# Optimization experiments

Hardware: AMD Instinct MI355X
Metric: run time of the kernel (lower is better)

## Reference

```python
import jax, jax.numpy as jnp
import numpy as np

N_NODES = 50000
N_EDGES = 800000
N_ENT = 500000
N_REL = 500
L = 2          # num_layers
H = 8          # head_num
D = 16         # per-head dim (hidden_dim // head_num)
HID = H * D    # 128
IN = 128       # in_ent_dim == in_rel_dim == hidden_dim
B = 64         # number of graphs in the batch
SLOPE = 0.2    # leaky-relu negative slope


def setup_inputs() -> dict:
    key = jax.random.key(0)
    ks = jax.random.split(key, 11)
    return {
        "ent_table": jax.random.normal(ks[0], (N_ENT, IN), jnp.float32) * 0.05,
        "rel_table": jax.random.normal(ks[1], (N_REL, IN), jnp.float32) * 0.05,
        "W_ent": jax.random.normal(ks[2], (L, IN, HID), jnp.float32) * 0.05,
        "W_rel": jax.random.normal(ks[3], (L, IN, HID), jnp.float32) * 0.05,
        "attn_l": jax.random.normal(ks[4], (L, H, D), jnp.float32) * 0.05,
        "attn_r": jax.random.normal(ks[5], (L, H, D), jnp.float32) * 0.05,
        "attn_e": jax.random.normal(ks[6], (L, H, D), jnp.float32) * 0.05,
        "ent_ids": jax.random.randint(ks[7], (N_NODES,), 0, N_ENT, jnp.int32),
        "rel_ids": jax.random.randint(ks[8], (N_EDGES,), 0, N_REL, jnp.int32),
        "src": jax.random.randint(ks[9], (N_EDGES,), 0, N_NODES, jnp.int32),
        "dst": jax.random.randint(ks[10], (N_EDGES,), 0, N_NODES, jnp.int32),
        # node-0 offset of each subgraph in the batched graph
        "graph_offsets": jnp.arange(B, dtype=jnp.int32) * (N_NODES // B),
    }


def _kge_layer(h, rel_f, src, dst, W_e, W_r, a_l, a_r, a_e):
    # GAT-style relation-aware message passing (KGELayer)
    feat = (h @ W_e).reshape(-1, H, D)        # [N,H,D]
    rfeat = (rel_f @ W_r).reshape(-1, H, D)   # [E,H,D]
    el = jnp.einsum('nhd,hd->nh', feat, a_l)  # src score
    er = jnp.einsum('nhd,hd->nh', feat, a_r)  # dst score
    ee = jnp.einsum('ehd,hd->eh', rfeat, a_e) # relation score
    e = jax.nn.leaky_relu(el[src] + er[dst] + ee, SLOPE)  # [E,H]
    # segment softmax over incoming edges of each dst node
    emax = jax.ops.segment_max(e, dst, num_segments=N_NODES)
    ex = jnp.exp(e - emax[dst])
    denom = jax.ops.segment_sum(ex, dst, num_segments=N_NODES)
    alpha = ex / denom[dst]                   # [E,H]
    msg = (feat[src] + rfeat) * alpha[:, :, None]  # [E,H,D]
    out = jax.ops.segment_sum(msg, dst, num_segments=N_NODES)  # [N,H,D]
    return out.reshape(-1, HID)


def reference(ent_table, rel_table, W_ent, W_rel, attn_l, attn_r, attn_e,
              ent_ids, rel_ids, src, dst, graph_offsets):
    h = ent_table[ent_ids]       # [N,IN]
    rel_f = rel_table[rel_ids]   # [E,IN]
    for l in range(L):
        h = _kge_layer(h, rel_f, src, dst, W_ent[l], W_rel[l],
                       attn_l[l], attn_r[l], attn_e[l])
    # CLS embedding: node 0 of each unbatched subgraph
    return h[graph_offsets]      # [B,HID]
```

## Files before the change

### kernel.cpp

```cpp
#include <hip/hip_runtime.h>
#include <hip/hip_bf16.h>


#define NN   50000
#define NE   800000
#define NR   500
#define HH   8
#define DD   16
#define HIDD 128
#define BB   64

#define MAXE2 16384
#define MAXS1 16448
#define MAXE1 262144
#define MAXS0 50000


__global__ void k_init(int* slot2, int* slot1, int* slot0, int* counters,
                       float* out2, float* den2) {
    int i = blockIdx.x * blockDim.x + threadIdx.x;
    int stride = gridDim.x * blockDim.x;
    for (int n = i; n < NN; n += stride) { slot2[n] = -1; slot1[n] = -1; slot0[n] = -1; }
    for (int n = i; n < BB * HIDD; n += stride) out2[n] = 0.f;
    for (int n = i; n < BB * HH; n += stride) den2[n] = 0.f;
    if (i < 8) counters[i] = 0;
}

__global__ void k_seed(const int* goffs, int* slot2, int* slot1, int* nodesS1,
                       int* counters) {
    int i = threadIdx.x;
    if (i < BB) {
        int n = goffs[i];
        slot2[n] = i;
        slot1[n] = -2;
        nodesS1[i] = n;
    }
    if (i == 0) counters[0] = BB;
}

#define EBUF 1024
#define NBUF 512
__global__ void k_scan(const int* __restrict__ src, const int* __restrict__ dst,
                       const int* __restrict__ slotHit, int* __restrict__ slotNew,
                       int* elist, int elistCap, int* nodes, int nodesCap,
                       int* counters, int cntE, int cntN) {
    __shared__ int lE[EBUF];
    __shared__ int lN[NBUF];
    __shared__ int cEsh, cNsh, baseE, baseN;
    if (threadIdx.x == 0) { cEsh = 0; cNsh = 0; }
    __syncthreads();
    int per = (NE + gridDim.x - 1) / gridDim.x;
    int lo = blockIdx.x * per;
    int hi = lo + per; if (hi > NE) hi = NE;
    for (int base = lo; base < hi; base += blockDim.x) {
        int e = base + threadIdx.x;
        if (e < hi) {
            int d = dst[e];
            if (slotHit[d] >= 0) {
                int pos = atomicAdd(&cEsh, 1);
                lE[pos] = e;
                int s = src[e];
                int old = atomicCAS(&slotNew[s], -1, -2);
                if (old == -1) {
                    int p2 = atomicAdd(&cNsh, 1);
                    lN[p2] = s;
                }
            }
        }
        __syncthreads();
        if (cEsh >= EBUF - 256 || cNsh >= NBUF - 256) {
            int nE = cEsh, nN = cNsh;
            if (threadIdx.x == 0) {
                baseE = atomicAdd(&counters[cntE], nE);
                baseN = atomicAdd(&counters[cntN], nN);
            }
            __syncthreads();
            for (int i = threadIdx.x; i < nE; i += blockDim.x) {
                int g = baseE + i; if (g < elistCap) elist[g] = lE[i];
            }
            for (int i = threadIdx.x; i < nN; i += blockDim.x) {
                int g = baseN + i; if (g < nodesCap) nodes[g] = lN[i];
            }
            __syncthreads();
            if (threadIdx.x == 0) { cEsh = 0; cNsh = 0; }
        }
        __syncthreads();
    }
    int nE = cEsh, nN = cNsh;
    if (threadIdx.x == 0) {
        baseE = atomicAdd(&counters[cntE], nE);
        baseN = atomicAdd(&counters[cntN], nN);
    }
    __syncthreads();
    for (int i = threadIdx.x; i < nE; i += blockDim.x) {
        int g = baseE + i; if (g < elistCap) elist[g] = lE[i];
    }
    for (int i = threadIdx.x; i < nN; i += blockDim.x) {
        int g = baseN + i; if (g < nodesCap) nodes[g] = lN[i];
    }
}

__global__ void k_finS1(int* slot1, const int* nodesS1, int* slot0, int* nodesS0,
                        int* counters) {
    int k = blockIdx.x * blockDim.x + threadIdx.x;
    int cnt = counters[0]; if (cnt > MAXS1) cnt = MAXS1;
    if (k < cnt) {
        int n = nodesS1[k];
        slot1[n] = k;
        slot0[n] = -2;
        nodesS0[k] = n;
    }
    if (k == 0) counters[1] = cnt;
}

__global__ void k_zeroS1(const int* counters, float* h1acc, float* den1) {
    int cnt = counters[0]; if (cnt > MAXS1) cnt = MAXS1;
    int i = blockIdx.x * blockDim.x + threadIdx.x;
    int stride = gridDim.x * blockDim.x;
    for (int n = i; n < cnt * HIDD; n += stride) h1acc[n] = 0.f;
    for (int n = i; n < cnt * HH; n += stride) den1[n] = 0.f;
}

__global__ void k_finS0(int* slot0, const int* nodesS0, const int* counters) {
    int k = blockIdx.x * blockDim.x + threadIdx.x;
    int cnt = counters[1]; if (cnt > MAXS0) cnt = MAXS0;
    if (k < cnt) slot0[nodesS0[k]] = k;
}

__global__ void k_rel(const float* rel_table, const float* __restrict__ W_rel,
                      const float* attn_e, float* rproj, float* ee) {
    int b = blockIdx.x;
    int l = b / NR, r = b % NR;
    int t = threadIdx.x;
    __shared__ float row[HIDD];
    __shared__ float rp[HIDD];
    row[t] = rel_table[r * HIDD + t];
    __syncthreads();
    const float* W = W_rel + l * HIDD * HIDD;
    float acc = 0.f;
    for (int j = 0; j < HIDD; j++) acc += row[j] * W[j * HIDD + t];
    rproj[(l * NR + r) * HIDD + t] = acc;
    rp[t] = acc;
    __syncthreads();
    if (t < HH) {
        float s = 0.f;
        for (int d = 0; d < DD; d++) s += rp[t * DD + d] * attn_e[(l * HH + t) * DD + d];
        ee[(l * NR + r) * HH + t] = s;
    }
}

#define FT 8
__global__ void k_feat0(const int* nodesS0, const int* counters, const int* ent_ids,
                        const float* __restrict__ ent_table, const float* __restrict__ W_ent,
                        const float* __restrict__ attn_l, const float* __restrict__ attn_r,
                        float* feat0, float* el0, float* er0) {
    int t = threadIdx.x;
    int cnt = counters[1]; if (cnt > MAXS0) cnt = MAXS0;
    __shared__ float rows[FT][HIDD];
    int nTiles = (cnt + FT - 1) / FT;
    for (int tile = blockIdx.x; tile < nTiles; tile += gridDim.x) {
        int k0 = tile * FT;
        #pragma unroll
        for (int m = 0; m < FT; m++) {
            int k = k0 + m;
            int n = nodesS0[k < cnt ? k : 0];
            rows[m][t] = ent_table[(long)ent_ids[n] * HIDD + t];
        }
        __syncthreads();
        float acc[FT];
        #pragma unroll
        for (int m = 0; m < FT; m++) acc[m] = 0.f;
        for (int j = 0; j < HIDD; j++) {
            float w = W_ent[j * HIDD + t];
            #pragma unroll
            for (int m = 0; m < FT; m++) acc[m] += rows[m][j] * w;
        }
        __syncthreads();
        #pragma unroll
        for (int m = 0; m < FT; m++) {
            int k = k0 + m;
            if (k < cnt) feat0[k * HIDD + t] = acc[m];
            rows[m][t] = acc[m];
        }
        __syncthreads();
        {
            int m = t >> 4, idx = t & 15, h = idx >> 1, isR = idx & 1;
            int k = k0 + m;
            if (k < cnt) {
                const float* av = (isR ? attn_r : attn_l) + h * DD;
                float s = 0.f;
                for (int d = 0; d < DD; d++) s += rows[m][h * DD + d] * av[d];
                if (isR) er0[k * HH + h] = s; else el0[k * HH + h] = s;
            }
        }
        __syncthreads();
    }
}

__global__ void k_score1(const int* e1list, const int* counters,
                         const int* src, const int* dst, const int* rel_ids,
                         const int* slot0, const int* slot1,
                         const float* el0, const float* er0, const float* ee0,
                         float* ex1, float* den1) {
    int i = blockIdx.x * blockDim.x + threadIdx.x;
    int stride = gridDim.x * blockDim.x;
    int cnt = counters[3]; if (cnt > MAXE1) cnt = MAXE1;
    int total = cnt * HH;
    for (; i < total; i += stride) {
        int eidx = i >> 3, h = i & 7;
        int e = e1list[eidx];
        int ks  = slot0[src[e]];
        int kd0 = slot0[dst[e]];
        int kd1 = slot1[dst[e]];
        int rid = rel_ids[e];
        float sc = el0[ks * HH + h] + er0[kd0 * HH + h] + ee0[rid * HH + h];
        sc = sc >= 0.f ? sc : 0.2f * sc;
        float ex = expf(sc);
        ex1[eidx * HH + h] = ex;
        atomicAdd(&den1[kd1 * HH + h], ex);
    }
}

__global__ void k_msg1(const int* e1list, const int* counters,
                       const int* src, const int* dst, const int* rel_ids,
                       const int* slot0, const int* slot1,
                       const float* __restrict__ feat0, const float* __restrict__ rproj0,
                       const float* __restrict__ ex1, float* h1acc) {
    int i = blockIdx.x * blockDim.x + threadIdx.x;
    int stride = gridDim.x * blockDim.x;
    int cnt = counters[3]; if (cnt > MAXE1) cnt = MAXE1;
    int total = cnt * HIDD;
    for (; i < total; i += stride) {
        int eidx = i >> 7, col = i & 127;
        int e = e1list[eidx];
        int ks  = slot0[src[e]];
        int kd  = slot1[dst[e]];
        int rid = rel_ids[e];
        float ex = ex1[eidx * HH + (col >> 4)];
        float v = (feat0[ks * HIDD + col] + rproj0[rid * HIDD + col]) * ex;
        atomicAdd(&h1acc[kd * HIDD + col], v);
    }
}

__global__ void k_feat1(const int* counters, const float* h1acc, const float* den1,
                        const float* __restrict__ W_ent1,
                        const float* attn_l1, const float* attn_r1,
                        float* feat1, float* el1, float* er1) {
    int t = threadIdx.x;
    int cnt = counters[0]; if (cnt > MAXS1) cnt = MAXS1;
    __shared__ float row[HIDD];
    __shared__ float f[HIDD];
    for (int k = blockIdx.x; k < cnt; k += gridDim.x) {
        float den = den1[k * HH + (t >> 4)];
        row[t] = den > 0.f ? h1acc[k * HIDD + t] / den : 0.f;
        __syncthreads();
        float acc = 0.f;
        for (int j = 0; j < HIDD; j++) acc += row[j] * W_ent1[j * HIDD + t];
        feat1[k * HIDD + t] = acc;
        f[t] = acc;
        __syncthreads();
        if (t < HH) {
            float s = 0.f;
            for (int d = 0; d < DD; d++) s += f[t * DD + d] * attn_l1[t * DD + d];
            el1[k * HH + t] = s;
        } else if (t < 2 * HH) {
            int h = t - HH;
            float s = 0.f;
            for (int d = 0; d < DD; d++) s += f[h * DD + d] * attn_r1[h * DD + d];
            er1[k * HH + h] = s;
        }
        __syncthreads();
    }
}

__global__ void k_score2(const int* e2list, const int* counters,
                         const int* src, const int* dst, const int* rel_ids,
                         const int* slot1, const int* slot2,
                         const float* el1, const float* er1, const float* ee1,
                         float* ex2, float* den2) {
    int i = blockIdx.x * blockDim.x + threadIdx.x;
    int stride = gridDim.x * blockDim.x;
    int cnt = counters[2]; if (cnt > MAXE2) cnt = MAXE2;
    int total = cnt * HH;
    for (; i < total; i += stride) {
        int eidx = i >> 3, h = i & 7;
        int e = e2list[eidx];
        int ks  = slot1[src[e]];
        int kd1 = slot1[dst[e]];
        int g   = slot2[dst[e]];
        int rid = rel_ids[e];
        float sc = el1[ks * HH + h] + er1[kd1 * HH + h] + ee1[rid * HH + h];
        sc = sc >= 0.f ? sc : 0.2f * sc;
        float ex = expf(sc);
        ex2[eidx * HH + h] = ex;
        atomicAdd(&den2[g * HH + h], ex);
    }
}

__global__ void k_msg2(const int* e2list, const int* counters,
                       const int* src, const int* dst, const int* rel_ids,
                       const int* slot1, const int* slot2,
                       const float* feat1, const float* rproj1, const float* ex2,
                       float* out2) {
    int i = blockIdx.x * blockDim.x + threadIdx.x;
    int stride = gridDim.x * blockDim.x;
    int cnt = counters[2]; if (cnt > MAXE2) cnt = MAXE2;
    int total = cnt * HIDD;
    for (; i < total; i += stride) {
        int eidx = i >> 7, col = i & 127;
        int e = e2list[eidx];
        int ks  = slot1[src[e]];
        int g   = slot2[dst[e]];
        int rid = rel_ids[e];
        float ex = ex2[eidx * HH + (col >> 4)];
        float v = (feat1[ks * HIDD + col] + rproj1[rid * HIDD + col]) * ex;
        atomicAdd(&out2[g * HIDD + col], v);
    }
}

__global__ void k_out(const float* out2, const float* den2, float* out) {
    int i = blockIdx.x * blockDim.x + threadIdx.x;
    if (i >= BB * HIDD) return;
    int g = i >> 7, col = i & 127;
    float den = den2[g * HH + (col >> 4)];
    out[i] = den > 0.f ? out2[i] / den : 0.f;
}

extern "C" void kernel_launch(void* const* d_in, const int* in_sizes, int n_in,
                              void* d_out, int out_size, void* d_ws, size_t ws_size,
                              hipStream_t stream) {
    const float* ent_table = (const float*)d_in[0];
    const float* rel_table = (const float*)d_in[1];
    const float* W_ent     = (const float*)d_in[2];
    const float* W_rel     = (const float*)d_in[3];
    const float* attn_l    = (const float*)d_in[4];
    const float* attn_r    = (const float*)d_in[5];
    const float* attn_e    = (const float*)d_in[6];
    const int*   ent_ids   = (const int*)d_in[7];
    const int*   rel_ids   = (const int*)d_in[8];
    const int*   src       = (const int*)d_in[9];
    const int*   dst       = (const int*)d_in[10];
    const int*   goffs     = (const int*)d_in[11];
    float*       out       = (float*)d_out;

    char* p = (char*)d_ws;
    auto alloc = [&](size_t nbytes) {
        void* q = (void*)p;
        p += (nbytes + 255) & ~(size_t)255;
        return q;
    };
    float* rproj   = (float*)alloc((size_t)2 * NR * HIDD * 4);
    float* ee      = (float*)alloc((size_t)2 * NR * HH * 4);
    int*   slot2   = (int*)alloc((size_t)NN * 4);
    int*   slot1   = (int*)alloc((size_t)NN * 4);
    int*   slot0   = (int*)alloc((size_t)NN * 4);
    int*   nodesS1 = (int*)alloc((size_t)MAXS1 * 4);
    int*   nodesS0 = (int*)alloc((size_t)MAXS0 * 4);
    int*   e2list  = (int*)alloc((size_t)MAXE2 * 4);
    int*   e1list  = (int*)alloc((size_t)MAXE1 * 4);
    int*   counters= (int*)alloc(8 * 4);
    float* feat0   = (float*)alloc((size_t)MAXS0 * HIDD * 4);
    float* el0     = (float*)alloc((size_t)MAXS0 * HH * 4);
    float* er0     = (float*)alloc((size_t)MAXS0 * HH * 4);
    float* ex1     = (float*)alloc((size_t)MAXE1 * HH * 4);
    float* h1acc   = (float*)alloc((size_t)MAXS1 * HIDD * 4);
    float* den1    = (float*)alloc((size_t)MAXS1 * HH * 4);
    float* feat1   = (float*)alloc((size_t)MAXS1 * HIDD * 4);
    float* el1     = (float*)alloc((size_t)MAXS1 * HH * 4);
    float* er1     = (float*)alloc((size_t)MAXS1 * HH * 4);
    float* ex2     = (float*)alloc((size_t)MAXE2 * HH * 4);
    float* out2    = (float*)alloc((size_t)BB * HIDD * 4);
    float* den2    = (float*)alloc((size_t)BB * HH * 4);

    const float* rproj0 = rproj;
    const float* rproj1 = rproj + (size_t)NR * HIDD;
    const float* ee0 = ee;
    const float* ee1 = ee + (size_t)NR * HH;
    const float* W_ent0 = W_ent;
    const float* W_ent1 = W_ent + HIDD * HIDD;
    const float* attn_l0 = attn_l, *attn_l1 = attn_l + HH * DD;
    const float* attn_r0 = attn_r, *attn_r1 = attn_r + HH * DD;

    hipLaunchKernelGGL(k_init, dim3(256), dim3(256), 0, stream,
                       slot2, slot1, slot0, counters, out2, den2);
    hipLaunchKernelGGL(k_seed, dim3(1), dim3(64), 0, stream,
                       goffs, slot2, slot1, nodesS1, counters);
    hipLaunchKernelGGL(k_scan, dim3(512), dim3(256), 0, stream,
                       src, dst, slot2, slot1, e2list, MAXE2, nodesS1, MAXS1,
                       counters, 2, 0);
    hipLaunchKernelGGL(k_finS1, dim3((MAXS1 + 255) / 256), dim3(256), 0, stream,
                       slot1, nodesS1, slot0, nodesS0, counters);
    hipLaunchKernelGGL(k_zeroS1, dim3(256), dim3(256), 0, stream,
                       counters, h1acc, den1);
    hipLaunchKernelGGL(k_scan, dim3(512), dim3(256), 0, stream,
                       src, dst, slot1, slot0, e1list, MAXE1, nodesS0, MAXS0,
                       counters, 3, 1);
    hipLaunchKernelGGL(k_finS0, dim3((MAXS0 + 255) / 256), dim3(256), 0, stream,
                       slot0, nodesS0, counters);
    hipLaunchKernelGGL(k_rel, dim3(2 * NR), dim3(HIDD), 0, stream,
                       rel_table, W_rel, attn_e, rproj, ee);
    hipLaunchKernelGGL(k_feat0, dim3(1024), dim3(HIDD), 0, stream,
                       nodesS0, counters, ent_ids, ent_table, W_ent0,
                       attn_l0, attn_r0, feat0, el0, er0);
    hipLaunchKernelGGL(k_score1, dim3(512), dim3(256), 0, stream,
                       e1list, counters, src, dst, rel_ids, slot0, slot1,
                       el0, er0, ee0, ex1, den1);
    hipLaunchKernelGGL(k_msg1, dim3(2048), dim3(256), 0, stream,
                       e1list, counters, src, dst, rel_ids, slot0, slot1,
                       feat0, rproj0, ex1, h1acc);
    hipLaunchKernelGGL(k_feat1, dim3(512), dim3(HIDD), 0, stream,
                       counters, h1acc, den1, W_ent1, attn_l1, attn_r1,
                       feat1, el1, er1);
    hipLaunchKernelGGL(k_score2, dim3(256), dim3(256), 0, stream,
                       e2list, counters, src, dst, rel_ids, slot1, slot2,
                       el1, er1, ee1, ex2, den2);
    hipLaunchKernelGGL(k_msg2, dim3(256), dim3(256), 0, stream,
                       e2list, counters, src, dst, rel_ids, slot1, slot2,
                       feat1, rproj1, ex2, out2);
    hipLaunchKernelGGL(k_out, dim3((BB * HIDD + 255) / 256), dim3(256), 0, stream,
                       out2, den2, out);
}
```

Measured before the change: 426.0 us.

## Build per-destination CSR and replace atomic scatter with pull-based fused layers

```diff
diff --git a/kernel.cpp b/kernel.cpp
--- a/kernel.cpp
+++ b/kernel.cpp
@@ -10,24 +10,23 @@
 #define HIDD 128
 #define BB   64
 
+#define GRIDS 1024
+#define PER   784
+
 #define MAXE2 16384
 #define MAXS1 16448
 #define MAXE1 262144
 #define MAXS0 50000
 
 
-__global__ void k_init(int* slot2, int* slot1, int* slot0, int* counters,
-                       float* out2, float* den2) {
+__global__ void k_init(int* slot2, int* slot1, int* slot0, int* counters) {
     int i = blockIdx.x * blockDim.x + threadIdx.x;
     int stride = gridDim.x * blockDim.x;
     for (int n = i; n < NN; n += stride) { slot2[n] = -1; slot1[n] = -1; slot0[n] = -1; }
-    for (int n = i; n < BB * HIDD; n += stride) out2[n] = 0.f;
-    for (int n = i; n < BB * HH; n += stride) den2[n] = 0.f;
     if (i < 8) counters[i] = 0;
 }
 
-__global__ void k_seed(const int* goffs, int* slot2, int* slot1, int* nodesS1,
-                       int* counters) {
+__global__ void k_seed(const int* goffs, int* slot2, int* slot1, int* nodesS1) {
     int i = threadIdx.x;
     if (i < BB) {
         int n = goffs[i];
@@ -35,130 +34,235 @@
         slot1[n] = -2;
         nodesS1[i] = n;
     }
-    if (i == 0) counters[0] = BB;
-}
-
-#define EBUF 1024
-#define NBUF 512
+}
+
 __global__ void k_scan(const int* __restrict__ src, const int* __restrict__ dst,
                        const int* __restrict__ slotHit, int* __restrict__ slotNew,
-                       int* elist, int elistCap, int* nodes, int nodesCap,
-                       int* counters, int cntE, int cntN) {
-    __shared__ int lE[EBUF];
-    __shared__ int lN[NBUF];
-    __shared__ int cEsh, cNsh, baseE, baseN;
-    if (threadIdx.x == 0) { cEsh = 0; cNsh = 0; }
-    __syncthreads();
-    int per = (NE + gridDim.x - 1) / gridDim.x;
-    int lo = blockIdx.x * per;
-    int hi = lo + per; if (hi > NE) hi = NE;
-    for (int base = lo; base < hi; base += blockDim.x) {
-        int e = base + threadIdx.x;
-        if (e < hi) {
-            int d = dst[e];
-            if (slotHit[d] >= 0) {
-                int pos = atomicAdd(&cEsh, 1);
-                lE[pos] = e;
-                int s = src[e];
-                int old = atomicCAS(&slotNew[s], -1, -2);
-                if (old == -1) {
-                    int p2 = atomicAdd(&cNsh, 1);
-                    lN[p2] = s;
-                }
+                       int* eseg, int* ecnt, int* nseg, int* ncnt) {
+    __shared__ int cE, cN;
+    if (threadIdx.x == 0) { cE = 0; cN = 0; }
+    __syncthreads();
+    int b = blockIdx.x;
+    int lo = b * PER;
+    int hi = lo + PER; if (hi > NE) hi = NE;
+    int* es = eseg + (size_t)b * PER;
+    int* ns = nseg + (size_t)b * PER;
+    for (int e = lo + threadIdx.x; e < hi; e += blockDim.x) {
+        int d = dst[e];
+        if (slotHit[d] >= 0) {
+            int pos = atomicAdd(&cE, 1);
+            es[pos] = e;
+            int s = src[e];
+            if (atomicCAS(&slotNew[s], -1, -2) == -1) {
+                int p = atomicAdd(&cN, 1);
+                ns[p] = s;
             }
         }
-        __syncthreads();
-        if (cEsh >= EBUF - 256 || cNsh >= NBUF - 256) {
-            int nE = cEsh, nN = cNsh;
-            if (threadIdx.x == 0) {
-                baseE = atomicAdd(&counters[cntE], nE);
-                baseN = atomicAdd(&counters[cntN], nN);
-            }
-            __syncthreads();
-            for (int i = threadIdx.x; i < nE; i += blockDim.x) {
-                int g = baseE + i; if (g < elistCap) elist[g] = lE[i];
-            }
-            for (int i = threadIdx.x; i < nN; i += blockDim.x) {
-                int g = baseN + i; if (g < nodesCap) nodes[g] = lN[i];
-            }
-            __syncthreads();
-            if (threadIdx.x == 0) { cEsh = 0; cNsh = 0; }
-        }
-        __syncthreads();
-    }
-    int nE = cEsh, nN = cNsh;
-    if (threadIdx.x == 0) {
-        baseE = atomicAdd(&counters[cntE], nE);
-        baseN = atomicAdd(&counters[cntN], nN);
-    }
-    __syncthreads();
-    for (int i = threadIdx.x; i < nE; i += blockDim.x) {
-        int g = baseE + i; if (g < elistCap) elist[g] = lE[i];
-    }
-    for (int i = threadIdx.x; i < nN; i += blockDim.x) {
-        int g = baseN + i; if (g < nodesCap) nodes[g] = lN[i];
-    }
-}
-
-__global__ void k_finS1(int* slot1, const int* nodesS1, int* slot0, int* nodesS0,
-                        int* counters) {
-    int k = blockIdx.x * blockDim.x + threadIdx.x;
-    int cnt = counters[0]; if (cnt > MAXS1) cnt = MAXS1;
-    if (k < cnt) {
-        int n = nodesS1[k];
-        slot1[n] = k;
-        slot0[n] = -2;
-        nodesS0[k] = n;
-    }
-    if (k == 0) counters[1] = cnt;
-}
-
-__global__ void k_zeroS1(const int* counters, float* h1acc, float* den1) {
-    int cnt = counters[0]; if (cnt > MAXS1) cnt = MAXS1;
+    }
+    __syncthreads();
+    if (threadIdx.x == 0) { ecnt[b] = cE; ncnt[b] = cN; }
+}
+
+__device__ int block_scan_counts(const int* cnts, int nblk, int* bases, int offset) {
+    __shared__ int part[256];
+    __shared__ int total_sh;
+    int t = threadIdx.x;
+    int per = (nblk + 255) / 256;
+    int s = 0;
+    for (int j = 0; j < per; j++) { int i = t * per + j; if (i < nblk) s += cnts[i]; }
+    part[t] = s;
+    __syncthreads();
+    for (int d = 1; d < 256; d <<= 1) {
+        int v = (t >= d) ? part[t - d] : 0;
+        __syncthreads();
+        part[t] += v;
+        __syncthreads();
+    }
+    int run = ((t == 0) ? 0 : part[t - 1]) + offset;
+    for (int j = 0; j < per; j++) {
+        int i = t * per + j;
+        if (i < nblk) { bases[i] = run; run += cnts[i]; }
+    }
+    if (t == 255) total_sh = part[255];
+    __syncthreads();
+    return total_sh;
+}
+
+__global__ void k_prefix2(const int* ecnt2, const int* ncnt2, int* ebase2, int* nbase2,
+                          int* counters, const int* nodesS1, int* slot1, int* slot0,
+                          int* nodesS0) {
+    int t = threadIdx.x;
+    int totE = block_scan_counts(ecnt2, GRIDS, ebase2, 0);
+    int totN = block_scan_counts(ncnt2, GRIDS, nbase2, BB);
+    if (t == 0) {
+        counters[2] = totE;
+        counters[0] = BB + totN;
+        counters[1] = BB + totN;
+    }
+    if (t < BB) {
+        int n = nodesS1[t];
+        slot1[n] = t;
+        slot0[n] = t;
+        nodesS0[t] = n;
+    }
+}
+
+__global__ void k_compact2(const int* eseg2, const int* ecnt2, const int* ebase2,
+                           const int* nseg2, const int* ncnt2, const int* nbase2,
+                           int* e2list, int* nodesS1, int* slot1, int* slot0,
+                           int* nodesS0, int* deg2) {
+    int b = blockIdx.x, t = threadIdx.x;
+    int ce = ecnt2[b], cn = ncnt2[b], be = ebase2[b], bn = nbase2[b];
+    const int* es = eseg2 + (size_t)b * PER;
+    const int* ns = nseg2 + (size_t)b * PER;
+    for (int i = t; i < ce; i += blockDim.x) {
+        int g = be + i; if (g < MAXE2) e2list[g] = es[i];
+    }
+    for (int i = t; i < cn; i += blockDim.x) {
+        int idx = bn + i;
+        if (idx < MAXS1) {
+            int n = ns[i];
+            nodesS1[idx] = n;
+            slot1[n] = idx;
+            slot0[n] = idx;
+            nodesS0[idx] = n;
+        }
+    }
+    if (b == 0) { for (int i = t; i < BB; i += blockDim.x) deg2[i] = 0; }
+}
+
+__global__ void k_prefix1(const int* ecnt1, const int* ncnt1, int* ebase1, int* nbase1,
+                          int* counters) {
+    int t = threadIdx.x;
+    int s0 = counters[1];
+    int totE = block_scan_counts(ecnt1, GRIDS, ebase1, 0);
+    int totN = block_scan_counts(ncnt1, GRIDS, nbase1, s0);
+    if (t == 0) {
+        counters[3] = totE;
+        counters[1] = s0 + totN;
+    }
+}
+
+__global__ void k_compact1(const int* eseg1, const int* ecnt1, const int* ebase1,
+                           const int* nseg1, const int* ncnt1, const int* nbase1,
+                           int* e1list, int* slot0, int* nodesS0,
+                           int* deg1, const int* counters) {
+    int b = blockIdx.x, t = threadIdx.x;
+    int ce = ecnt1[b], cn = ncnt1[b], be = ebase1[b], bn = nbase1[b];
+    const int* es = eseg1 + (size_t)b * PER;
+    const int* ns = nseg1 + (size_t)b * PER;
+    for (int i = t; i < ce; i += blockDim.x) {
+        int g = be + i; if (g < MAXE1) e1list[g] = es[i];
+    }
+    for (int i = t; i < cn; i += blockDim.x) {
+        int idx = bn + i;
+        if (idx < MAXS0) {
+            int n = ns[i];
+            slot0[n] = idx;
+            nodesS0[idx] = n;
+        }
+    }
+    int cnt1 = counters[0]; if (cnt1 > MAXS1) cnt1 = MAXS1;
+    for (int i = b * blockDim.x + t; i < cnt1; i += gridDim.x * blockDim.x) deg1[i] = 0;
+}
+
+__global__ void k_hist(const int* e2list, const int* e1list, const int* counters,
+                       const int* dst, const int* slot2, const int* slot1,
+                       int* deg2, int* deg1) {
     int i = blockIdx.x * blockDim.x + threadIdx.x;
     int stride = gridDim.x * blockDim.x;
-    for (int n = i; n < cnt * HIDD; n += stride) h1acc[n] = 0.f;
-    for (int n = i; n < cnt * HH; n += stride) den1[n] = 0.f;
-}
-
-__global__ void k_finS0(int* slot0, const int* nodesS0, const int* counters) {
-    int k = blockIdx.x * blockDim.x + threadIdx.x;
+    int c2 = counters[2]; if (c2 > MAXE2) c2 = MAXE2;
+    int c1 = counters[3]; if (c1 > MAXE1) c1 = MAXE1;
+    for (int k = i; k < c2; k += stride) atomicAdd(&deg2[slot2[dst[e2list[k]]]], 1);
+    for (int k = i; k < c1; k += stride) atomicAdd(&deg1[slot1[dst[e1list[k]]]], 1);
+}
+
+__device__ void excl_scan_glob(const int* deg, int n, int* rp) {
+    __shared__ int part[256];
+    int t = threadIdx.x;
+    int per = (n + 255) / 256;
+    int s = 0;
+    for (int j = 0; j < per; j++) { int i = t * per + j; if (i < n) s += deg[i]; }
+    part[t] = s;
+    __syncthreads();
+    for (int d = 1; d < 256; d <<= 1) {
+        int v = (t >= d) ? part[t - d] : 0;
+        __syncthreads();
+        part[t] += v;
+        __syncthreads();
+    }
+    int run = (t == 0) ? 0 : part[t - 1];
+    for (int j = 0; j < per; j++) {
+        int i = t * per + j;
+        if (i < n) { rp[i] = run; run += deg[i]; }
+    }
+    if (t == 255) rp[n] = part[255];
+    __syncthreads();
+}
+
+__global__ void k_rowptr(const int* deg2, const int* deg1, const int* counters,
+                         int* rp2, int* rp1, int* cur2, int* cur1) {
+    int t = threadIdx.x;
+    int cnt1 = counters[0]; if (cnt1 > MAXS1) cnt1 = MAXS1;
+    excl_scan_glob(deg2, BB, rp2);
+    excl_scan_glob(deg1, cnt1, rp1);
+    for (int i = t; i < BB; i += blockDim.x) cur2[i] = rp2[i];
+    for (int i = t; i < cnt1; i += blockDim.x) cur1[i] = rp1[i];
+}
+
+__global__ void k_scatter(const int* e2list, const int* e1list, const int* counters,
+                          const int* dst, const int* slot2, const int* slot1,
+                          int* cur2, int* cur1, int* csr2, int* csr1) {
+    int i = blockIdx.x * blockDim.x + threadIdx.x;
+    int stride = gridDim.x * blockDim.x;
+    int c2 = counters[2]; if (c2 > MAXE2) c2 = MAXE2;
+    int c1 = counters[3]; if (c1 > MAXE1) c1 = MAXE1;
+    for (int k = i; k < c2; k += stride) {
+        int e = e2list[k];
+        int pos = atomicAdd(&cur2[slot2[dst[e]]], 1);
+        if (pos < MAXE2) csr2[pos] = e;
+    }
+    for (int k = i; k < c1; k += stride) {
+        int e = e1list[k];
+        int pos = atomicAdd(&cur1[slot1[dst[e]]], 1);
+        if (pos < MAXE1) csr1[pos] = e;
+    }
+}
+
+#define FT 8
+__global__ void k_relfeat0(const float* rel_table, const float* __restrict__ W_rel,
+                           const float* attn_e, float* rproj, float* ee,
+                           const int* nodesS0, const int* counters, const int* ent_ids,
+                           const float* __restrict__ ent_table,
+                           const float* __restrict__ W_ent,
+                           const float* __restrict__ attn_l,
+                           const float* __restrict__ attn_r,
+                           float* feat0, float* el0, float* er0) {
+    __shared__ float rows[FT][HIDD];
+    int t = threadIdx.x;
+    if (blockIdx.x < 2 * NR) {
+        int l = blockIdx.x / NR, r = blockIdx.x % NR;
+        rows[0][t] = rel_table[r * HIDD + t];
+        __syncthreads();
+        const float* W = W_rel + l * HIDD * HIDD;
+        float acc = 0.f;
+        for (int j = 0; j < HIDD; j++) acc += rows[0][j] * W[j * HIDD + t];
+        rproj[(l * NR + r) * HIDD + t] = acc;
+        rows[1][t] = acc;
+        __syncthreads();
+        if (t < HH) {
+            float s = 0.f;
+            for (int d = 0; d < DD; d++)
+                s += rows[1][t * DD + d] * attn_e[(l * HH + t) * DD + d];
+            ee[(l * NR + r) * HH + t] = s;
+        }
+        return;
+    }
     int cnt = counters[1]; if (cnt > MAXS0) cnt = MAXS0;
-    if (k < cnt) slot0[nodesS0[k]] = k;
-}
-
-__global__ void k_rel(const float* rel_table, const float* __restrict__ W_rel,
-                      const float* attn_e, float* rproj, float* ee) {
-    int b = blockIdx.x;
-    int l = b / NR, r = b % NR;
-    int t = threadIdx.x;
-    __shared__ float row[HIDD];
-    __shared__ float rp[HIDD];
-    row[t] = rel_table[r * HIDD + t];
-    __syncthreads();
-    const float* W = W_rel + l * HIDD * HIDD;
-    float acc = 0.f;
-    for (int j = 0; j < HIDD; j++) acc += row[j] * W[j * HIDD + t];
-    rproj[(l * NR + r) * HIDD + t] = acc;
-    rp[t] = acc;
-    __syncthreads();
-    if (t < HH) {
-        float s = 0.f;
-        for (int d = 0; d < DD; d++) s += rp[t * DD + d] * attn_e[(l * HH + t) * DD + d];
-        ee[(l * NR + r) * HH + t] = s;
-    }
-}
-
-#define FT 8
-__global__ void k_feat0(const int* nodesS0, const int* counters, const int* ent_ids,
-                        const float* __restrict__ ent_table, const float* __restrict__ W_ent,
-                        const float* __restrict__ attn_l, const float* __restrict__ attn_r,
-                        float* feat0, float* el0, float* er0) {
-    int t = threadIdx.x;
-    int cnt = counters[1]; if (cnt > MAXS0) cnt = MAXS0;
-    __shared__ float rows[FT][HIDD];
+    int tile0 = blockIdx.x - 2 * NR;
+    int tstride = gridDim.x - 2 * NR;
     int nTiles = (cnt + FT - 1) / FT;
-    for (int tile = blockIdx.x; tile < nTiles; tile += gridDim.x) {
+    for (int tile = tile0; tile < nTiles; tile += tstride) {
         int k0 = tile * FT;
         #pragma unroll
         for (int m = 0; m < FT; m++) {
@@ -197,133 +301,77 @@
     }
 }
 
-__global__ void k_score1(const int* e1list, const int* counters,
-                         const int* src, const int* dst, const int* rel_ids,
-                         const int* slot0, const int* slot1,
-                         const float* el0, const float* er0, const float* ee0,
-                         float* ex1, float* den1) {
-    int i = blockIdx.x * blockDim.x + threadIdx.x;
-    int stride = gridDim.x * blockDim.x;
-    int cnt = counters[3]; if (cnt > MAXE1) cnt = MAXE1;
-    int total = cnt * HH;
-    for (; i < total; i += stride) {
-        int eidx = i >> 3, h = i & 7;
-        int e = e1list[eidx];
-        int ks  = slot0[src[e]];
-        int kd0 = slot0[dst[e]];
-        int kd1 = slot1[dst[e]];
-        int rid = rel_ids[e];
-        float sc = el0[ks * HH + h] + er0[kd0 * HH + h] + ee0[rid * HH + h];
-        sc = sc >= 0.f ? sc : 0.2f * sc;
-        float ex = expf(sc);
-        ex1[eidx * HH + h] = ex;
-        atomicAdd(&den1[kd1 * HH + h], ex);
-    }
-}
-
-__global__ void k_msg1(const int* e1list, const int* counters,
-                       const int* src, const int* dst, const int* rel_ids,
-                       const int* slot0, const int* slot1,
-                       const float* __restrict__ feat0, const float* __restrict__ rproj0,
-                       const float* __restrict__ ex1, float* h1acc) {
-    int i = blockIdx.x * blockDim.x + threadIdx.x;
-    int stride = gridDim.x * blockDim.x;
-    int cnt = counters[3]; if (cnt > MAXE1) cnt = MAXE1;
-    int total = cnt * HIDD;
-    for (; i < total; i += stride) {
-        int eidx = i >> 7, col = i & 127;
-        int e = e1list[eidx];
-        int ks  = slot0[src[e]];
-        int kd  = slot1[dst[e]];
-        int rid = rel_ids[e];
-        float ex = ex1[eidx * HH + (col >> 4)];
-        float v = (feat0[ks * HIDD + col] + rproj0[rid * HIDD + col]) * ex;
-        atomicAdd(&h1acc[kd * HIDD + col], v);
-    }
-}
-
-__global__ void k_feat1(const int* counters, const float* h1acc, const float* den1,
-                        const float* __restrict__ W_ent1,
-                        const float* attn_l1, const float* attn_r1,
-                        float* feat1, float* el1, float* er1) {
-    int t = threadIdx.x;
-    int cnt = counters[0]; if (cnt > MAXS1) cnt = MAXS1;
+__global__ void k_layer1(const int* counters, const int* rp1, const int* csr1,
+                         const int* src, const int* rel_ids, const int* slot0,
+                         const float* __restrict__ el0, const float* __restrict__ er0,
+                         const float* __restrict__ ee0,
+                         const float* __restrict__ feat0, const float* __restrict__ rproj0,
+                         const float* __restrict__ W_ent1,
+                         const float* attn_l1, const float* attn_r1,
+                         float* feat1, float* el1, float* er1) {
+    int cnt1 = counters[0]; if (cnt1 > MAXS1) cnt1 = MAXS1;
+    int t = threadIdx.x;
+    int h = t >> 4;
     __shared__ float row[HIDD];
-    __shared__ float f[HIDD];
-    for (int k = blockIdx.x; k < cnt; k += gridDim.x) {
-        float den = den1[k * HH + (t >> 4)];
-        row[t] = den > 0.f ? h1acc[k * HIDD + t] / den : 0.f;
-        __syncthreads();
-        float acc = 0.f;
-        for (int j = 0; j < HIDD; j++) acc += row[j] * W_ent1[j * HIDD + t];
-        feat1[k * HIDD + t] = acc;
-        f[t] = acc;
+    __shared__ float f2[HIDD];
+    for (int k = blockIdx.x; k < cnt1; k += gridDim.x) {
+        int lo = rp1[k], hi = rp1[k + 1];
+        float er_k = er0[k * HH + h];
+        float acc = 0.f, sumex = 0.f;
+        for (int i = lo; i < hi; i++) {
+            int e = csr1[i];
+            int ks = slot0[src[e]];
+            int rid = rel_ids[e];
+            float sc = el0[ks * HH + h] + er_k + ee0[rid * HH + h];
+            sc = sc >= 0.f ? sc : 0.2f * sc;
+            float ex = __expf(sc);
+            sumex += ex;
+            acc += ex * (feat0[ks * HIDD + t] + rproj0[rid * HIDD + t]);
+        }
+        row[t] = (hi > lo) ? acc / sumex : 0.f;
+        __syncthreads();
+        float f = 0.f;
+        for (int j = 0; j < HIDD; j++) f += row[j] * W_ent1[j * HIDD + t];
+        feat1[k * HIDD + t] = f;
+        f2[t] = f;
         __syncthreads();
         if (t < HH) {
             float s = 0.f;
-            for (int d = 0; d < DD; d++) s += f[t * DD + d] * attn_l1[t * DD + d];
+            for (int d = 0; d < DD; d++) s += f2[t * DD + d] * attn_l1[t * DD + d];
             el1[k * HH + t] = s;
         } else if (t < 2 * HH) {
-            int h = t - HH;
+            int hh = t - HH;
             float s = 0.f;
-            for (int d = 0; d < DD; d++) s += f[h * DD + d] * attn_r1[h * DD + d];
-            er1[k * HH + h] = s;
-        }
-        __syncthreads();
-    }
-}
-
-__global__ void k_score2(const int* e2list, const int* counters,
-                         const int* src, const int* dst, const int* rel_ids,
-                         const int* slot1, const int* slot2,
-                         const float* el1, const float* er1, const float* ee1,
-                         float* ex2, float* den2) {
-    int i = blockIdx.x * blockDim.x + threadIdx.x;
-    int stride = gridDim.x * blockDim.x;
-    int cnt = counters[2]; if (cnt > MAXE2) cnt = MAXE2;
-    int total = cnt * HH;
-    for (; i < total; i += stride) {
-        int eidx = i >> 3, h = i & 7;
-        int e = e2list[eidx];
-        int ks  = slot1[src[e]];
-        int kd1 = slot1[dst[e]];
-        int g   = slot2[dst[e]];
+            for (int d = 0; d < DD; d++) s += f2[hh * DD + d] * attn_r1[hh * DD + d];
+            er1[k * HH + hh] = s;
+        }
+        __syncthreads();
+    }
+}
+
+__global__ void k_layer2(const int* rp2, const int* csr2,
+                         const int* src, const int* rel_ids, const int* slot1,
+                         const float* __restrict__ el1, const float* __restrict__ er1,
+                         const float* __restrict__ ee1,
+                         const float* __restrict__ feat1, const float* __restrict__ rproj1,
+                         float* out) {
+    int g = blockIdx.x;
+    int t = threadIdx.x;
+    int h = t >> 4;
+    int lo = rp2[g], hi = rp2[g + 1];
+    float er_g = er1[g * HH + h];
+    float acc = 0.f, sumex = 0.f;
+    for (int i = lo; i < hi; i++) {
+        int e = csr2[i];
+        int ks = slot1[src[e]];
         int rid = rel_ids[e];
-        float sc = el1[ks * HH + h] + er1[kd1 * HH + h] + ee1[rid * HH + h];
+        float sc = el1[ks * HH + h] + er_g + ee1[rid * HH + h];
         sc = sc >= 0.f ? sc : 0.2f * sc;
-        float ex = expf(sc);
-        ex2[eidx * HH + h] = ex;
-        atomicAdd(&den2[g * HH + h], ex);
-    }
-}
-
-__global__ void k_msg2(const int* e2list, const int* counters,
-                       const int* src, const int* dst, const int* rel_ids,
-                       const int* slot1, const int* slot2,
-                       const float* feat1, const float* rproj1, const float* ex2,
-                       float* out2) {
-    int i = blockIdx.x * blockDim.x + threadIdx.x;
-    int stride = gridDim.x * blockDim.x;
-    int cnt = counters[2]; if (cnt > MAXE2) cnt = MAXE2;
-    int total = cnt * HIDD;
-    for (; i < total; i += stride) {
-        int eidx = i >> 7, col = i & 127;
-        int e = e2list[eidx];
-        int ks  = slot1[src[e]];
-        int g   = slot2[dst[e]];
-        int rid = rel_ids[e];
-        float ex = ex2[eidx * HH + (col >> 4)];
-        float v = (feat1[ks * HIDD + col] + rproj1[rid * HIDD + col]) * ex;
-        atomicAdd(&out2[g * HIDD + col], v);
-    }
-}
-
-__global__ void k_out(const float* out2, const float* den2, float* out) {
-    int i = blockIdx.x * blockDim.x + threadIdx.x;
-    if (i >= BB * HIDD) return;
-    int g = i >> 7, col = i & 127;
-    float den = den2[g * HH + (col >> 4)];
-    out[i] = den > 0.f ? out2[i] / den : 0.f;
+        float ex = __expf(sc);
+        sumex += ex;
+        acc += ex * (feat1[ks * HIDD + t] + rproj1[rid * HIDD + t]);
+    }
+    out[g * HIDD + t] = (hi > lo) ? acc / sumex : 0.f;
 }
 
 extern "C" void kernel_launch(void* const* d_in, const int* in_sizes, int n_in,
@@ -359,18 +407,32 @@
     int*   e2list  = (int*)alloc((size_t)MAXE2 * 4);
     int*   e1list  = (int*)alloc((size_t)MAXE1 * 4);
     int*   counters= (int*)alloc(8 * 4);
+    int*   eseg2   = (int*)alloc((size_t)GRIDS * PER * 4);
+    int*   nseg2   = (int*)alloc((size_t)GRIDS * PER * 4);
+    int*   eseg1   = (int*)alloc((size_t)GRIDS * PER * 4);
+    int*   nseg1   = (int*)alloc((size_t)GRIDS * PER * 4);
+    int*   ecnt2   = (int*)alloc((size_t)GRIDS * 4);
+    int*   ncnt2   = (int*)alloc((size_t)GRIDS * 4);
+    int*   ecnt1   = (int*)alloc((size_t)GRIDS * 4);
+    int*   ncnt1   = (int*)alloc((size_t)GRIDS * 4);
+    int*   ebase2  = (int*)alloc((size_t)GRIDS * 4);
+    int*   nbase2  = (int*)alloc((size_t)GRIDS * 4);
+    int*   ebase1  = (int*)alloc((size_t)GRIDS * 4);
+    int*   nbase1  = (int*)alloc((size_t)GRIDS * 4);
+    int*   deg2    = (int*)alloc((size_t)BB * 4);
+    int*   rp2     = (int*)alloc((size_t)(BB + 1) * 4);
+    int*   cur2    = (int*)alloc((size_t)BB * 4);
+    int*   deg1    = (int*)alloc((size_t)MAXS1 * 4);
+    int*   rp1     = (int*)alloc((size_t)(MAXS1 + 1) * 4);
+    int*   cur1    = (int*)alloc((size_t)MAXS1 * 4);
+    int*   csr2    = (int*)alloc((size_t)MAXE2 * 4);
+    int*   csr1    = (int*)alloc((size_t)MAXE1 * 4);
     float* feat0   = (float*)alloc((size_t)MAXS0 * HIDD * 4);
     float* el0     = (float*)alloc((size_t)MAXS0 * HH * 4);
     float* er0     = (float*)alloc((size_t)MAXS0 * HH * 4);
-    float* ex1     = (float*)alloc((size_t)MAXE1 * HH * 4);
-    float* h1acc   = (float*)alloc((size_t)MAXS1 * HIDD * 4);
-    float* den1    = (float*)alloc((size_t)MAXS1 * HH * 4);
     float* feat1   = (float*)alloc((size_t)MAXS1 * HIDD * 4);
     float* el1     = (float*)alloc((size_t)MAXS1 * HH * 4);
     float* er1     = (float*)alloc((size_t)MAXS1 * HH * 4);
-    float* ex2     = (float*)alloc((size_t)MAXE2 * HH * 4);
-    float* out2    = (float*)alloc((size_t)BB * HIDD * 4);
-    float* den2    = (float*)alloc((size_t)BB * HH * 4);
 
     const float* rproj0 = rproj;
     const float* rproj1 = rproj + (size_t)NR * HIDD;
@@ -382,41 +444,40 @@
     const float* attn_r0 = attn_r, *attn_r1 = attn_r + HH * DD;
 
     hipLaunchKernelGGL(k_init, dim3(256), dim3(256), 0, stream,
-                       slot2, slot1, slot0, counters, out2, den2);
+                       slot2, slot1, slot0, counters);
     hipLaunchKernelGGL(k_seed, dim3(1), dim3(64), 0, stream,
-                       goffs, slot2, slot1, nodesS1, counters);
-    hipLaunchKernelGGL(k_scan, dim3(512), dim3(256), 0, stream,
-                       src, dst, slot2, slot1, e2list, MAXE2, nodesS1, MAXS1,
-                       counters, 2, 0);
-    hipLaunchKernelGGL(k_finS1, dim3((MAXS1 + 255) / 256), dim3(256), 0, stream,
-                       slot1, nodesS1, slot0, nodesS0, counters);
-    hipLaunchKernelGGL(k_zeroS1, dim3(256), dim3(256), 0, stream,
-                       counters, h1acc, den1);
-    hipLaunchKernelGGL(k_scan, dim3(512), dim3(256), 0, stream,
-                       src, dst, slot1, slot0, e1list, MAXE1, nodesS0, MAXS0,
-                       counters, 3, 1);
-    hipLaunchKernelGGL(k_finS0, dim3((MAXS0 + 255) / 256), dim3(256), 0, stream,
-                       slot0, nodesS0, counters);
-    hipLaunchKernelGGL(k_rel, dim3(2 * NR), dim3(HIDD), 0, stream,
-                       rel_table, W_rel, attn_e, rproj, ee);
-    hipLaunchKernelGGL(k_feat0, dim3(1024), dim3(HIDD), 0, stream,
+                       goffs, slot2, slot1, nodesS1);
+    hipLaunchKernelGGL(k_scan, dim3(GRIDS), dim3(256), 0, stream,
+                       src, dst, slot2, slot1, eseg2, ecnt2, nseg2, ncnt2);
+    hipLaunchKernelGGL(k_prefix2, dim3(1), dim3(256), 0, stream,
+                       ecnt2, ncnt2, ebase2, nbase2, counters,
+                       nodesS1, slot1, slot0, nodesS0);
+    hipLaunchKernelGGL(k_compact2, dim3(GRIDS), dim3(256), 0, stream,
+                       eseg2, ecnt2, ebase2, nseg2, ncnt2, nbase2,
+                       e2list, nodesS1, slot1, slot0, nodesS0, deg2);
+    hipLaunchKernelGGL(k_scan, dim3(GRIDS), dim3(256), 0, stream,
+                       src, dst, slot1, slot0, eseg1, ecnt1, nseg1, ncnt1);
+    hipLaunchKernelGGL(k_prefix1, dim3(1), dim3(256), 0, stream,
+                       ecnt1, ncnt1, ebase1, nbase1, counters);
+    hipLaunchKernelGGL(k_compact1, dim3(GRIDS), dim3(256), 0, stream,
+                       eseg1, ecnt1, ebase1, nseg1, ncnt1, nbase1,
+                       e1list, slot0, nodesS0, deg1, counters);
+    hipLaunchKernelGGL(k_hist, dim3(256), dim3(256), 0, stream,
+                       e2list, e1list, counters, dst, slot2, slot1, deg2, deg1);
+    hipLaunchKernelGGL(k_rowptr, dim3(1), dim3(256), 0, stream,
+                       deg2, deg1, counters, rp2, rp1, cur2, cur1);
+    hipLaunchKernelGGL(k_scatter, dim3(256), dim3(256), 0, stream,
+                       e2list, e1list, counters, dst, slot2, slot1,
+                       cur2, cur1, csr2, csr1);
+    hipLaunchKernelGGL(k_relfeat0, dim3(2 * NR + 1024), dim3(HIDD), 0, stream,
+                       rel_table, W_rel, attn_e, rproj, ee,
                        nodesS0, counters, ent_ids, ent_table, W_ent0,
                        attn_l0, attn_r0, feat0, el0, er0);
-    hipLaunchKernelGGL(k_score1, dim3(512), dim3(256), 0, stream,
-                       e1list, counters, src, dst, rel_ids, slot0, slot1,
-                       el0, er0, ee0, ex1, den1);
-    hipLaunchKernelGGL(k_msg1, dim3(2048), dim3(256), 0, stream,
-                       e1list, counters, src, dst, rel_ids, slot0, slot1,
-                       feat0, rproj0, ex1, h1acc);
-    hipLaunchKernelGGL(k_feat1, dim3(512), dim3(HIDD), 0, stream,
-                       counters, h1acc, den1, W_ent1, attn_l1, attn_r1,
-                       feat1, el1, er1);
-    hipLaunchKernelGGL(k_score2, dim3(256), dim3(256), 0, stream,
-                       e2list, counters, src, dst, rel_ids, slot1, slot2,
-                       el1, er1, ee1, ex2, den2);
-    hipLaunchKernelGGL(k_msg2, dim3(256), dim3(256), 0, stream,
-                       e2list, counters, src, dst, rel_ids, slot1, slot2,
-                       feat1, rproj1, ex2, out2);
-    hipLaunchKernelGGL(k_out, dim3((BB * HIDD + 255) / 256), dim3(256), 0, stream,
-                       out2, den2, out);
-}
+    hipLaunchKernelGGL(k_layer1, dim3(2048), dim3(HIDD), 0, stream,
+                       counters, rp1, csr1, src, rel_ids, slot0,
+                       el0, er0, ee0, feat0, rproj0, W_ent1,
+                       attn_l1, attn_r1, feat1, el1, er1);
+    hipLaunchKernelGGL(k_layer2, dim3(BB), dim3(HIDD), 0, stream,
+                       rp2, csr2, src, rel_ids, slot1,
+                       el1, er1, ee1, feat1, rproj1, out);
+}
```

Result: slower. 436.3 us (+2.4%).
